# Kernel tuning notes

Hardware: AMD Instinct MI355X
Metric: run time of the kernel (lower is better)

Reference implementation:

```python
import jax, jax.numpy as jnp
import numpy as np

N_NODES = 100000
N_EDGES = 1600000
IN_DIM = 128
HID = 128
OUT_DIM = 64
N_LAYERS = 2
MAXK = 16


def setup_inputs() -> dict:
    key = jax.random.key(0)
    ks = jax.random.split(key, 8)
    x = jax.random.normal(ks[0], (N_NODES, IN_DIM), dtype=jnp.float32)
    src = jax.random.randint(ks[1], (N_EDGES,), 0, N_NODES, dtype=jnp.int32)
    dst = jax.random.randint(ks[2], (N_EDGES,), 0, N_NODES, dtype=jnp.int32)
    # Linear weights stored as [in, out] (y = x @ W + b), xavier-like scale
    s_in = float(np.sqrt(2.0 / (IN_DIM + HID)))
    s_h = float(np.sqrt(2.0 / (HID + HID)))
    s_out = float(np.sqrt(2.0 / (HID + OUT_DIM)))
    W_in = jax.random.normal(ks[3], (IN_DIM, HID), dtype=jnp.float32) * s_in
    b_in = jnp.zeros((HID,), dtype=jnp.float32)
    W_lin = jax.random.normal(ks[4], (N_LAYERS, HID, HID), dtype=jnp.float32) * s_h
    b_lin = jnp.zeros((N_LAYERS, HID), dtype=jnp.float32)
    eps = jnp.zeros((N_LAYERS,), dtype=jnp.float32)  # learn_eps=True, init_eps=0
    W_out = jax.random.normal(ks[5], (HID, OUT_DIM), dtype=jnp.float32) * s_out
    b_out = jnp.zeros((OUT_DIM,), dtype=jnp.float32)
    return {"x": x, "src": src, "dst": dst, "W_in": W_in, "b_in": b_in,
            "W_lin": W_lin, "b_lin": b_lin, "eps": eps,
            "W_out": W_out, "b_out": b_out}


def _maxk(x, k):
    # OPTMaxK: keep top-k entries per row (dim=1), zero the rest.
    _, idx = jax.lax.top_k(x, k)                      # [N, k]
    rows = jnp.arange(x.shape[0])[:, None]            # [N, 1]
    mask = jnp.zeros_like(x).at[rows, idx].set(1.0)
    return x * mask


def reference(x, src, dst, W_in, b_in, W_lin, b_lin, eps, W_out, b_out):
    n = x.shape[0]
    h = jax.nn.relu(x @ W_in + b_in)                  # lin_in + relu
    for i in range(N_LAYERS):
        h = h @ W_lin[i] + b_lin[i]                   # per-layer Linear
        h_sparse = _maxk(h, MAXK)                     # MaxK nonlinearity (dropout p=0 -> identity)
        # GIN sum aggregation over edges: neigh[v] = sum_{(u->v)} h_sparse[u]
        msg = jnp.take(h_sparse, src, axis=0)         # [E, HID] irregular gather
        neigh = jax.ops.segment_sum(msg, dst, num_segments=n)
        h = (1.0 + eps[i]) * h_sparse + neigh         # eps residual (apply_func=None, no norm)
    return h @ W_out + b_out
```

## Files before the change

kernel.cpp:

```cpp
#include <hip/hip_runtime.h>
#include <cstdint>
#include <cstddef>


typedef __attribute__((ext_vector_type(8))) short bf16x8;
typedef __attribute__((ext_vector_type(4))) float f32x4;

#define BSHIFT 8
#define NBUK 512

__device__ __forceinline__ unsigned rne_bf16(float v) {
  unsigned u = __float_as_uint(v);
  return (u + 0x7fffu + ((u >> 16) & 1u)) >> 16;
}

__device__ __forceinline__ void row_select16(
    const float v[8], int row, int nrows, int shift, int s, unsigned below,
    unsigned char* __restrict__ Cs, float* __restrict__ Vs) {
  unsigned k[8];
#pragma unroll
  for (int j = 0; j < 8; ++j) {
    const unsigned u = __float_as_uint(v[j]);
    k[j] = u ^ (((unsigned)((int)u >> 31)) | 0x80000000u);
  }

  unsigned P = 0;
  int kth = 16;
  int sz = 128;
  bool done = false;
  for (int b = 31; b >= 0; --b) {
    const unsigned tgt = (P >> b) | 1u;
    int c = 0;
#pragma unroll
    for (int j = 0; j < 8; ++j) {
      const unsigned long long bal = __ballot((k[j] >> b) == tgt);
      c += __popc((unsigned)((bal >> shift) & 0xFFFFull));
    }
    if (!done) {
      if (c >= kth) {
        P |= (1u << b);
        sz = c;
      } else {
        sz -= c;
        kth -= c;
      }
      done = (sz == kth);
    }
    if (__all(done)) break;
  }
  if (done) P -= 1u;

  unsigned gtm[8], eqm[8];
  int gt_total = 0;
#pragma unroll
  for (int j = 0; j < 8; ++j) {
    const unsigned long long gb = __ballot(k[j] > P);
    const unsigned long long eb = __ballot(k[j] == P);
    gtm[j] = (unsigned)((gb >> shift) & 0xFFFFull);
    eqm[j] = (unsigned)((eb >> shift) & 0xFFFFull);
    gt_total += __popc(gtm[j]);
  }
  const int need = 16 - gt_total;
  int gt_pre = 0, eq_pre = 0;
#pragma unroll
  for (int j = 0; j < 8; ++j) {
    const bool isgt = k[j] > P;
    const bool iseq = k[j] == P;
    const int gtb = gt_pre + __popc(gtm[j] & below);
    const int eqb = eq_pre + __popc(eqm[j] & below);
    if (row < nrows && (isgt || (iseq && eqb < need))) {
      const int rank = gtb + (isgt ? min(eqb, need) : eqb);
      Vs[(size_t)row * 16 + rank] = v[j];
      Cs[(size_t)row * 16 + rank] = (unsigned char)(j * 16 + s);
    }
    gt_pre += __popc(gtm[j]);
    eq_pre += __popc(eqm[j]);
  }
}

__global__ __launch_bounds__(256) void wt_build_all_kernel(
    const float* __restrict__ W_in, const float* __restrict__ W_lin,
    const float* __restrict__ W_out, short* __restrict__ out) {
  const int i = blockIdx.x * 256 + threadIdx.x;
  if (i >= 57344) return;
  const float* W;
  int nout, local;
  short* H;
  if (i < 16384) {
    W = W_in; nout = 128; local = i; H = out;
  } else if (i < 32768) {
    W = W_lin; nout = 128; local = i - 16384; H = out + 32768;
  } else if (i < 49152) {
    W = W_lin + 16384; nout = 128; local = i - 32768; H = out + 65536;
  } else {
    W = W_out; nout = 64; local = i - 49152; H = out + 98304;
  }
  const int nn = local >> 7, k = local & 127;
  const float v = W[k * nout + nn];
  const unsigned hb = rne_bf16(v);
  const float hf = __uint_as_float(hb << 16);
  const unsigned lb = rne_bf16(v - hf);
  H[local] = (short)hb;
  H[local + nout * 128] = (short)lb;
}

__global__ __launch_bounds__(256, 2) void gemm_in_kernel(
    const float* __restrict__ X, const short* __restrict__ WtH,
    const short* __restrict__ WtL, const float* __restrict__ bias,
    short* __restrict__ Yh, short* __restrict__ Yl, int nrows, int ntiles) {
  constexpr int NOUT = 128;
  constexpr int NT = NOUT / 16;
  constexpr int LDB = 128 * 2 + 16;
  constexpr int PLANE = NOUT * LDB;
  __shared__ char lds[2 * PLANE];

  const int tid = threadIdx.x;
  for (int u = tid; u < 2 * NOUT * 16; u += 256) {
    const int plane = u / (NOUT * 16);
    const int v = u % (NOUT * 16);
    const int nrow = v >> 4, seg = v & 15;
    const short* src = plane ? WtL : WtH;
    const float4 d = *(const float4*)&src[nrow * 128 + seg * 8];
    *(float4*)&lds[plane * PLANE + nrow * LDB + seg * 16] = d;
  }
  __syncthreads();

  const int lane = tid & 63;
  const int wv = tid >> 6;
  const int li = lane & 15;
  const int kg = lane >> 4;

  float bv[NT];
#pragma unroll
  for (int t = 0; t < NT; ++t) bv[t] = bias[t * 16 + li];

  for (int tile = blockIdx.x; tile < ntiles; tile += gridDim.x) {
    const int rowbase = tile * 256 + wv * 64;

    f32x4 acc[4][NT];
#pragma unroll
    for (int rg = 0; rg < 4; ++rg)
#pragma unroll
      for (int t = 0; t < NT; ++t) acc[rg][t] = (f32x4){0.f, 0.f, 0.f, 0.f};

#pragma unroll
    for (int c = 0; c < 4; ++c) {
      bf16x8 ah[4], al[4];
#pragma unroll
      for (int rg = 0; rg < 4; ++rg) {
        const int row = rowbase + rg * 16 + li;
        const int rowc = (row < nrows) ? row : (nrows - 1);
        const float* xrow = X + (size_t)rowc * 128 + c * 32 + kg * 8;
        const float4 p0 = *(const float4*)&xrow[0];
        const float4 p1 = *(const float4*)&xrow[4];
        const float f[8] = {p0.x, p0.y, p0.z, p0.w, p1.x, p1.y, p1.z, p1.w};
#pragma unroll
        for (int e = 0; e < 8; ++e) {
          const unsigned hb = rne_bf16(f[e]);
          const float hf = __uint_as_float(hb << 16);
          ah[rg][e] = (short)hb;
          al[rg][e] = (short)rne_bf16(f[e] - hf);
        }
      }
      const int kb = c * 64 + kg * 16;
#pragma unroll
      for (int t = 0; t < NT; ++t) {
        const int boff = (t * 16 + li) * LDB + kb;
        const bf16x8 bh = *(const bf16x8*)&lds[boff];
        const bf16x8 bl = *(const bf16x8*)&lds[PLANE + boff];
#pragma unroll
        for (int rg = 0; rg < 4; ++rg) {
          acc[rg][t] =
              __builtin_amdgcn_mfma_f32_16x16x32_bf16(al[rg], bh, acc[rg][t], 0, 0, 0);
          acc[rg][t] =
              __builtin_amdgcn_mfma_f32_16x16x32_bf16(ah[rg], bl, acc[rg][t], 0, 0, 0);
          acc[rg][t] =
              __builtin_amdgcn_mfma_f32_16x16x32_bf16(ah[rg], bh, acc[rg][t], 0, 0, 0);
        }
      }
    }

#pragma unroll
    for (int rg = 0; rg < 4; ++rg) {
      const int orow = rowbase + rg * 16 + kg * 4;
#pragma unroll
      for (int t = 0; t < NT; ++t) {
        const int col = t * 16 + li;
#pragma unroll
        for (int r = 0; r < 4; ++r) {
          const int rr = orow + r;
          if (rr < nrows) {
            const float o = fmaxf(acc[rg][t][r] + bv[t], 0.f);
            const unsigned hb = rne_bf16(o);
            const float hf = __uint_as_float(hb << 16);
            Yh[(size_t)rr * 128 + col] = (short)hb;
            Yl[(size_t)rr * 128 + col] = (short)rne_bf16(o - hf);
          }
        }
      }
    }
  }
}

__global__ __launch_bounds__(256, 2) void gemm_maxk_kernel(
    const short* __restrict__ Xh, const short* __restrict__ Xl,
    const short* __restrict__ WtH, const short* __restrict__ WtL,
    const float* __restrict__ bias, unsigned char* __restrict__ Cs,
    float* __restrict__ Vs, int nrows, int ntiles) {
  constexpr int NOUT = 128;
  constexpr int NT = NOUT / 16;
  constexpr int LDB = 128 * 2 + 16;
  constexpr int PLANE = NOUT * LDB;
  __shared__ char lds[2 * PLANE];

  const int tid = threadIdx.x;
  for (int u = tid; u < 2 * NOUT * 16; u += 256) {
    const int plane = u / (NOUT * 16);
    const int v = u % (NOUT * 16);
    const int nrow = v >> 4, seg = v & 15;
    const short* src = plane ? WtL : WtH;
    const float4 d = *(const float4*)&src[nrow * 128 + seg * 8];
    *(float4*)&lds[plane * PLANE + nrow * LDB + seg * 16] = d;
  }
  __syncthreads();

  const int lane = tid & 63;
  const int wv = tid >> 6;
  const int li = lane & 15;
  const int kg = lane >> 4;
  const int shift = kg * 16;
  const unsigned below = (1u << li) - 1u;

  float bv[NT];
#pragma unroll
  for (int t = 0; t < NT; ++t) bv[t] = bias[t * 16 + li];

  for (int tile = blockIdx.x; tile < ntiles; tile += gridDim.x) {
    const int rowbase = tile * 256 + wv * 64;

    f32x4 acc[4][NT];
#pragma unroll
    for (int rg = 0; rg < 4; ++rg)
#pragma unroll
      for (int t = 0; t < NT; ++t) acc[rg][t] = (f32x4){0.f, 0.f, 0.f, 0.f};

#pragma unroll
    for (int c = 0; c < 4; ++c) {
      bf16x8 ah[4], al[4];
#pragma unroll
      for (int rg = 0; rg < 4; ++rg) {
        const int row = rowbase + rg * 16 + li;
        const int rowc = (row < nrows) ? row : (nrows - 1);
        ah[rg] = *(const bf16x8*)&Xh[(size_t)rowc * 128 + c * 32 + kg * 8];
        al[rg] = *(const bf16x8*)&Xl[(size_t)rowc * 128 + c * 32 + kg * 8];
      }
      const int kb = c * 64 + kg * 16;
#pragma unroll
      for (int t = 0; t < NT; ++t) {
        const int boff = (t * 16 + li) * LDB + kb;
        const bf16x8 bh = *(const bf16x8*)&lds[boff];
        const bf16x8 bl = *(const bf16x8*)&lds[PLANE + boff];
#pragma unroll
        for (int rg = 0; rg < 4; ++rg) {
          acc[rg][t] =
              __builtin_amdgcn_mfma_f32_16x16x32_bf16(al[rg], bh, acc[rg][t], 0, 0, 0);
          acc[rg][t] =
              __builtin_amdgcn_mfma_f32_16x16x32_bf16(ah[rg], bl, acc[rg][t], 0, 0, 0);
          acc[rg][t] =
              __builtin_amdgcn_mfma_f32_16x16x32_bf16(ah[rg], bh, acc[rg][t], 0, 0, 0);
        }
      }
    }

#pragma unroll
    for (int rg = 0; rg < 4; ++rg) {
#pragma unroll
      for (int r = 0; r < 4; ++r) {
        const int row = rowbase + rg * 16 + kg * 4 + r;
        float v[8];
#pragma unroll
        for (int t = 0; t < NT; ++t) v[t] = acc[rg][t][r] + bv[t];
        row_select16(v, row, nrows, shift, li, below, Cs, Vs);
      }
    }
  }
}

template <int NOUT>
__global__ __launch_bounds__(256, 2) void gemm_pl_kernel(
    const short* __restrict__ Xh, const short* __restrict__ Xl,
    const short* __restrict__ WtH, const short* __restrict__ WtL,
    const float* __restrict__ bias, float* __restrict__ Y, int nrows,
    int ntiles) {
  constexpr int NT = NOUT / 16;
  constexpr int LDB = 128 * 2 + 16;
  constexpr int PLANE = NOUT * LDB;
  __shared__ char lds[2 * PLANE];

  const int tid = threadIdx.x;
  for (int u = tid; u < 2 * NOUT * 16; u += 256) {
    const int plane = u / (NOUT * 16);
    const int v = u % (NOUT * 16);
    const int nrow = v >> 4, seg = v & 15;
    const short* src = plane ? WtL : WtH;
    const float4 d = *(const float4*)&src[nrow * 128 + seg * 8];
    *(float4*)&lds[plane * PLANE + nrow * LDB + seg * 16] = d;
  }
  __syncthreads();

  const int lane = tid & 63;
  const int wv = tid >> 6;
  const int li = lane & 15;
  const int kg = lane >> 4;

  float bv[NT];
#pragma unroll
  for (int t = 0; t < NT; ++t) bv[t] = bias[t * 16 + li];

  for (int tile = blockIdx.x; tile < ntiles; tile += gridDim.x) {
    const int rowbase = tile * 256 + wv * 64;

    f32x4 acc[4][NT];
#pragma unroll
    for (int rg = 0; rg < 4; ++rg)
#pragma unroll
      for (int t = 0; t < NT; ++t) acc[rg][t] = (f32x4){0.f, 0.f, 0.f, 0.f};

#pragma unroll
    for (int c = 0; c < 4; ++c) {
      bf16x8 ah[4], al[4];
#pragma unroll
      for (int rg = 0; rg < 4; ++rg) {
        const int row = rowbase + rg * 16 + li;
        const int rowc = (row < nrows) ? row : (nrows - 1);
        ah[rg] = *(const bf16x8*)&Xh[(size_t)rowc * 128 + c * 32 + kg * 8];
        al[rg] = *(const bf16x8*)&Xl[(size_t)rowc * 128 + c * 32 + kg * 8];
      }
      const int kb = c * 64 + kg * 16;
#pragma unroll
      for (int t = 0; t < NT; ++t) {
        const int boff = (t * 16 + li) * LDB + kb;
        const bf16x8 bh = *(const bf16x8*)&lds[boff];
        const bf16x8 bl = *(const bf16x8*)&lds[PLANE + boff];
#pragma unroll
        for (int rg = 0; rg < 4; ++rg) {
          acc[rg][t] =
              __builtin_amdgcn_mfma_f32_16x16x32_bf16(al[rg], bh, acc[rg][t], 0, 0, 0);
          acc[rg][t] =
              __builtin_amdgcn_mfma_f32_16x16x32_bf16(ah[rg], bl, acc[rg][t], 0, 0, 0);
          acc[rg][t] =
              __builtin_amdgcn_mfma_f32_16x16x32_bf16(ah[rg], bh, acc[rg][t], 0, 0, 0);
        }
      }
    }

#pragma unroll
    for (int rg = 0; rg < 4; ++rg) {
      const int orow = rowbase + rg * 16 + kg * 4;
#pragma unroll
      for (int t = 0; t < NT; ++t) {
        const int col = t * 16 + li;
#pragma unroll
        for (int r = 0; r < 4; ++r) {
          const int rr = orow + r;
          if (rr < nrows) Y[(size_t)rr * NOUT + col] = acc[rg][t][r] + bv[t];
        }
      }
    }
  }
}

__global__ __launch_bounds__(256) void bhist_kernel(const int* __restrict__ dst,
                                                    int* __restrict__ BC,
                                                    int E) {
  __shared__ int bh[NBUK];
  for (int i = threadIdx.x; i < NBUK; i += 256) bh[i] = 0;
  __syncthreads();
  const int stride = gridDim.x * 256;
  for (int e = blockIdx.x * 256 + threadIdx.x; e < E; e += stride)
    atomicAdd(&bh[dst[e] >> BSHIFT], 1);
  __syncthreads();
  for (int i = threadIdx.x; i < NBUK; i += 256)
    if (bh[i]) atomicAdd(&BC[i], bh[i]);
}

__global__ __launch_bounds__(NBUK) void bscan_kernel(
    const int* __restrict__ BC, int* __restrict__ bases,
    int* __restrict__ bcur, int* __restrict__ rs, int n, int E) {
  __shared__ int sc[NBUK];
  const int t = threadIdx.x;
  const int c = BC[t];
  sc[t] = c;
  __syncthreads();
  for (int st = 1; st < NBUK; st <<= 1) {
    const int v = sc[t];
    const int u = (t >= st) ? sc[t - st] : 0;
    __syncthreads();
    sc[t] = v + u;
    __syncthreads();
  }
  const int excl = sc[t] - c;
  bases[t] = excl;
  bcur[t] = excl;
  if (t == 0) rs[n] = E;
}

__global__ __launch_bounds__(256) void bin_kernel(
    const int* __restrict__ src, const int* __restrict__ dst,
    int* __restrict__ bcur, uint2* __restrict__ binned, int E, int chunk) {
  __shared__ int cnt[NBUK], off[NBUK], gbase[NBUK];
  __shared__ unsigned short bktof[4096];
  __shared__ uint2 buf[4096];
  const int t = threadIdx.x;
  const int beg = blockIdx.x * chunk;
  const int m = min(chunk, E - beg);
  if (m <= 0) return;

  for (int i = t; i < NBUK; i += 256) cnt[i] = 0;
  __syncthreads();

  int d[16], s[16], lp[16], bk[16];
#pragma unroll
  for (int i = 0; i < 16; ++i) {
    const int j = i * 256 + t;
    if (j < m) {
      d[i] = dst[beg + j];
      s[i] = src[beg + j];
      bk[i] = d[i] >> BSHIFT;
      lp[i] = atomicAdd(&cnt[bk[i]], 1);
    } else {
      bk[i] = -1;
    }
  }
  __syncthreads();

  for (int i = t; i < NBUK; i += 256) off[i] = cnt[i];
  __syncthreads();
  for (int st = 1; st < NBUK; st <<= 1) {
    int v0, v1, u0, u1;
    {
      const int i0 = t, i1 = t + 256;
      v0 = off[i0]; u0 = (i0 >= st) ? off[i0 - st] : 0;
      v1 = off[i1]; u1 = (i1 >= st) ? off[i1 - st] : 0;
    }
    __syncthreads();
    off[t] = v0 + u0;
    off[t + 256] = v1 + u1;
    __syncthreads();
  }

  for (int i = t; i < NBUK; i += 256) {
    const int c = cnt[i];
    if (c > 0) {
      gbase[i] = atomicAdd(&bcur[i], c);
      const int e0 = off[i] - c;
      for (int k = 0; k < c; ++k) bktof[e0 + k] = (unsigned short)i;
    }
  }
  __syncthreads();

#pragma unroll
  for (int i = 0; i < 16; ++i) {
    if (bk[i] >= 0) {
      buf[(off[bk[i]] - cnt[bk[i]]) + lp[i]] =
          make_uint2((unsigned)d[i], (unsigned)s[i]);
    }
  }
  __syncthreads();

  for (int j = t; j < m; j += 256) {
    const int b = bktof[j];
    const int e0 = off[b] - cnt[b];
    binned[gbase[b] + (j - e0)] = buf[j];
  }
}

__global__ __launch_bounds__(256) void bbuild_kernel(
    const int* __restrict__ bases, const int* __restrict__ BC,
    const uint2* __restrict__ binned, int* __restrict__ rs,
    int* __restrict__ csr_src, int n) {
  __shared__ int nd[256], sc[256], cur[256];
  const int b = blockIdx.x;
  const int t = threadIdx.x;
  const int base = bases[b];
  const int count = BC[b];
  const int node0 = b << BSHIFT;

  nd[t] = 0;
  __syncthreads();
  for (int i = t; i < count; i += 256)
    atomicAdd(&nd[binned[base + i].x & 255], 1);
  __syncthreads();

  sc[t] = nd[t];
  __syncthreads();
  for (int st = 1; st < 256; st <<= 1) {
    const int v = sc[t];
    const int u = (t >= st) ? sc[t - st] : 0;
    __syncthreads();
    sc[t] = v + u;
    __syncthreads();
  }
  const int excl = sc[t] - nd[t];
  cur[t] = excl;
  if (node0 + t < n) rs[node0 + t] = base + excl;
  __syncthreads();

  for (int i = t; i < count; i += 256) {
    const uint2 p = binned[base + i];
    const int pos = atomicAdd(&cur[p.x & 255], 1);
    csr_src[base + pos] = (int)p.y;
  }
}

__global__ __launch_bounds__(256) void gather6_kernel(
    const int* __restrict__ rs, const int* __restrict__ csr_src,
    const unsigned char* __restrict__ Cs, const float* __restrict__ Vs,
    const float* __restrict__ eps_p, short* __restrict__ Ah,
    short* __restrict__ Al, int nrows) {
  __shared__ __align__(16) float sv[4][16][16];
  __shared__ __align__(16) unsigned char scb[4][16][16];
  __shared__ float accb[4][4 * 132];
  const int lane = threadIdx.x & 63;
  const int wid = threadIdx.x >> 6;
  const float e1 = 1.0f + *eps_p;
  const int ee = lane >> 2;
  const int q = lane & 3;
  const int g = lane >> 4;
  const int p = lane & 15;
  float* acc = accb[wid];
  float4* acc4 = (float4*)acc;

  for (int r = blockIdx.x * 4 + wid; r < nrows; r += gridDim.x * 4) {
    for (int i = lane; i < 132; i += 64)
      acc4[i] = make_float4(0.f, 0.f, 0.f, 0.f);

    const int beg = rs[r], end = rs[r + 1];
    for (int base = beg; base < end; base += 16) {
      const int cnt = min(16, end - base);
      if (ee < cnt) {
        const int s = csr_src[base + ee];
        if (q == 0) {
          const int4 c4 = *(const int4*)&Cs[(size_t)s * 16];
          *(int4*)&scb[wid][ee][0] = c4;
        }
        const float4 v = *(const float4*)&Vs[(size_t)s * 16 + q * 4];
        *(float4*)&sv[wid][ee][q * 4] = v;
      }
      for (int e = 0; e < cnt; e += 4) {
        const int eg = e + g;
        if (eg < cnt) {
          const int col = scb[wid][eg][p];
          const float val = sv[wid][eg][p];
          acc[g * 132 + col] += val;
        }
      }
    }
    if (lane < 16) {
      const int c = Cs[(size_t)r * 16 + lane];
      const float v = Vs[(size_t)r * 16 + lane];
      acc[c] += e1 * v;
    }
    const float a0 = acc[lane] + acc[132 + lane] + acc[264 + lane] +
                     acc[396 + lane];
    const float a1 = acc[64 + lane] + acc[132 + 64 + lane] +
                     acc[264 + 64 + lane] + acc[396 + 64 + lane];
    const unsigned h0 = rne_bf16(a0);
    const unsigned h1 = rne_bf16(a1);
    Ah[(size_t)r * 128 + lane] = (short)h0;
    Ah[(size_t)r * 128 + 64 + lane] = (short)h1;
    Al[(size_t)r * 128 + lane] =
        (short)rne_bf16(a0 - __uint_as_float(h0 << 16));
    Al[(size_t)r * 128 + 64 + lane] =
        (short)rne_bf16(a1 - __uint_as_float(h1 << 16));
  }
}

extern "C" void kernel_launch(void* const* d_in, const int* in_sizes, int n_in,
                              void* d_out, int out_size, void* d_ws,
                              size_t ws_size, hipStream_t stream) {
  const float* x = (const float*)d_in[0];
  const int* src = (const int*)d_in[1];
  const int* dst = (const int*)d_in[2];
  const float* W_in = (const float*)d_in[3];
  const float* b_in = (const float*)d_in[4];
  const float* W_lin = (const float*)d_in[5];
  const float* b_lin = (const float*)d_in[6];
  const float* eps = (const float*)d_in[7];
  const float* W_out = (const float*)d_in[8];
  const float* b_out = (const float*)d_in[9];
  float* out = (float*)d_out;

  const int n = in_sizes[0] / 128;
  const int E = in_sizes[1];

  char* w = (char*)d_ws;
  unsigned char* Cs = (unsigned char*)w; w += (size_t)n * 16;
  float* Vs = (float*)w;              w += (size_t)n * 16 * 4;
  int* rs = (int*)w;                  w += (size_t)(n + 1) * 4;
  int* csr_src = (int*)w;             w += (size_t)E * 4;
  uint2* binned = (uint2*)w;          w += (size_t)E * 8;
  int* BC = (int*)w;                  w += NBUK * 4;
  int* bases = (int*)w;               w += NBUK * 4;
  int* bcur = (int*)w;                w += NBUK * 4;
  short* wtAll = (short*)w;           w += (size_t)114688 * 2;
  short* Ah = (short*)w;              w += (size_t)n * 128 * 2;
  short* Al = (short*)w;              w += (size_t)n * 128 * 2;

  short* wtIn = wtAll;
  short* wtL0 = wtAll + 32768;
  short* wtL1 = wtAll + 65536;
  short* wtOut = wtAll + 98304;

  const int ptiles = (n + 255) / 256;
  const int nbuk_eff = (n + 255) >> BSHIFT;
  const int chunk = 4000;
  const int cblocks = (E + chunk - 1) / chunk;
  const dim3 blk(256);

  hipMemsetAsync(BC, 0, NBUK * 4, stream);
  bhist_kernel<<<256, blk, 0, stream>>>(dst, BC, E);
  bscan_kernel<<<1, NBUK, 0, stream>>>(BC, bases, bcur, rs, n, E);
  bin_kernel<<<cblocks, blk, 0, stream>>>(src, dst, bcur, binned, E, chunk);
  bbuild_kernel<<<nbuk_eff, blk, 0, stream>>>(bases, BC, binned, rs, csr_src,
                                              n);

  wt_build_all_kernel<<<(57344 + 255) / 256, blk, 0, stream>>>(W_in, W_lin,
                                                               W_out, wtAll);

  gemm_in_kernel<<<ptiles, blk, 0, stream>>>(x, wtIn, wtIn + 16384, b_in, Ah,
                                             Al, n, ptiles);

  for (int l = 0; l < 2; ++l) {
    short* wt = l ? wtL1 : wtL0;
    gemm_maxk_kernel<<<ptiles, blk, 0, stream>>>(
        Ah, Al, wt, wt + 16384, b_lin + (size_t)l * 128, Cs, Vs, n, ptiles);
    gather6_kernel<<<2048, blk, 0, stream>>>(rs, csr_src, Cs, Vs, eps + l, Ah,
                                             Al, n);
  }

  gemm_pl_kernel<64><<<ptiles, blk, 0, stream>>>(Ah, Al, wtOut, wtOut + 8192,
                                                 b_out, out, n, ptiles);
}
```

Measured before the change: 441.9 us.

## Split fused GEMM+MaxK into separate GEMM and standalone top-k select kernels

Replaces the fused per-layer GEMM with in-register top-16 selection by a plain GEMM that writes a full fp32 activation buffer, followed by a dedicated maxk_kernel that reads it back and performs the ballot-based radix select. Layer 1 uses a new 512-thread GEMM variant with 32 rows per wave. The aim is to free the GEMM from the register pressure and divergence of the select loop and run selection at its own occupancy. In exchange it adds an extra kernel launch and an n×128 fp32 round trip through global memory per layer.

```diff
diff --git a/kernel.cpp b/kernel.cpp
--- a/kernel.cpp
+++ b/kernel.cpp
@@ -12,70 +12,6 @@
 __device__ __forceinline__ unsigned rne_bf16(float v) {
   unsigned u = __float_as_uint(v);
   return (u + 0x7fffu + ((u >> 16) & 1u)) >> 16;
-}
-
-__device__ __forceinline__ void row_select16(
-    const float v[8], int row, int nrows, int shift, int s, unsigned below,
-    unsigned char* __restrict__ Cs, float* __restrict__ Vs) {
-  unsigned k[8];
-#pragma unroll
-  for (int j = 0; j < 8; ++j) {
-    const unsigned u = __float_as_uint(v[j]);
-    k[j] = u ^ (((unsigned)((int)u >> 31)) | 0x80000000u);
-  }
-
-  unsigned P = 0;
-  int kth = 16;
-  int sz = 128;
-  bool done = false;
-  for (int b = 31; b >= 0; --b) {
-    const unsigned tgt = (P >> b) | 1u;
-    int c = 0;
-#pragma unroll
-    for (int j = 0; j < 8; ++j) {
-      const unsigned long long bal = __ballot((k[j] >> b) == tgt);
-      c += __popc((unsigned)((bal >> shift) & 0xFFFFull));
-    }
-    if (!done) {
-      if (c >= kth) {
-        P |= (1u << b);
-        sz = c;
-      } else {
-        sz -= c;
-        kth -= c;
-      }
-      done = (sz == kth);
-    }
-    if (__all(done)) break;
-  }
-  if (done) P -= 1u;
-
-  unsigned gtm[8], eqm[8];
-  int gt_total = 0;
-#pragma unroll
-  for (int j = 0; j < 8; ++j) {
-    const unsigned long long gb = __ballot(k[j] > P);
-    const unsigned long long eb = __ballot(k[j] == P);
-    gtm[j] = (unsigned)((gb >> shift) & 0xFFFFull);
-    eqm[j] = (unsigned)((eb >> shift) & 0xFFFFull);
-    gt_total += __popc(gtm[j]);
-  }
-  const int need = 16 - gt_total;
-  int gt_pre = 0, eq_pre = 0;
-#pragma unroll
-  for (int j = 0; j < 8; ++j) {
-    const bool isgt = k[j] > P;
-    const bool iseq = k[j] == P;
-    const int gtb = gt_pre + __popc(gtm[j] & below);
-    const int eqb = eq_pre + __popc(eqm[j] & below);
-    if (row < nrows && (isgt || (iseq && eqb < need))) {
-      const int rank = gtb + (isgt ? min(eqb, need) : eqb);
-      Vs[(size_t)row * 16 + rank] = v[j];
-      Cs[(size_t)row * 16 + rank] = (unsigned char)(j * 16 + s);
-    }
-    gt_pre += __popc(gtm[j]);
-    eq_pre += __popc(eqm[j]);
-  }
 }
 
 __global__ __launch_bounds__(256) void wt_build_all_kernel(
@@ -165,9 +101,8 @@
       const int kb = c * 64 + kg * 16;
 #pragma unroll
       for (int t = 0; t < NT; ++t) {
-        const int boff = (t * 16 + li) * LDB + kb;
-        const bf16x8 bh = *(const bf16x8*)&lds[boff];
-        const bf16x8 bl = *(const bf16x8*)&lds[PLANE + boff];
+        const bf16x8 bh = *(const bf16x8*)&lds[(t * 16 + li) * LDB + kb];
+        const bf16x8 bl = *(const bf16x8*)&lds[PLANE + (t * 16 + li) * LDB + kb];
 #pragma unroll
         for (int rg = 0; rg < 4; ++rg) {
           acc[rg][t] =
@@ -197,90 +132,6 @@
             Yl[(size_t)rr * 128 + col] = (short)rne_bf16(o - hf);
           }
         }
-      }
-    }
-  }
-}
-
-__global__ __launch_bounds__(256, 2) void gemm_maxk_kernel(
-    const short* __restrict__ Xh, const short* __restrict__ Xl,
-    const short* __restrict__ WtH, const short* __restrict__ WtL,
-    const float* __restrict__ bias, unsigned char* __restrict__ Cs,
-    float* __restrict__ Vs, int nrows, int ntiles) {
-  constexpr int NOUT = 128;
-  constexpr int NT = NOUT / 16;
-  constexpr int LDB = 128 * 2 + 16;
-  constexpr int PLANE = NOUT * LDB;
-  __shared__ char lds[2 * PLANE];
-
-  const int tid = threadIdx.x;
-  for (int u = tid; u < 2 * NOUT * 16; u += 256) {
-    const int plane = u / (NOUT * 16);
-    const int v = u % (NOUT * 16);
-    const int nrow = v >> 4, seg = v & 15;
-    const short* src = plane ? WtL : WtH;
-    const float4 d = *(const float4*)&src[nrow * 128 + seg * 8];
-    *(float4*)&lds[plane * PLANE + nrow * LDB + seg * 16] = d;
-  }
-  __syncthreads();
-
-  const int lane = tid & 63;
-  const int wv = tid >> 6;
-  const int li = lane & 15;
-  const int kg = lane >> 4;
-  const int shift = kg * 16;
-  const unsigned below = (1u << li) - 1u;
-
-  float bv[NT];
-#pragma unroll
-  for (int t = 0; t < NT; ++t) bv[t] = bias[t * 16 + li];
-
-  for (int tile = blockIdx.x; tile < ntiles; tile += gridDim.x) {
-    const int rowbase = tile * 256 + wv * 64;
-
-    f32x4 acc[4][NT];
-#pragma unroll
-    for (int rg = 0; rg < 4; ++rg)
-#pragma unroll
-      for (int t = 0; t < NT; ++t) acc[rg][t] = (f32x4){0.f, 0.f, 0.f, 0.f};
-
-#pragma unroll
-    for (int c = 0; c < 4; ++c) {
-      bf16x8 ah[4], al[4];
-#pragma unroll
-      for (int rg = 0; rg < 4; ++rg) {
-        const int row = rowbase + rg * 16 + li;
-        const int rowc = (row < nrows) ? row : (nrows - 1);
-        ah[rg] = *(const bf16x8*)&Xh[(size_t)rowc * 128 + c * 32 + kg * 8];
-        al[rg] = *(const bf16x8*)&Xl[(size_t)rowc * 128 + c * 32 + kg * 8];
-      }
-      const int kb = c * 64 + kg * 16;
-#pragma unroll
-      for (int t = 0; t < NT; ++t) {
-        const int boff = (t * 16 + li) * LDB + kb;
-        const bf16x8 bh = *(const bf16x8*)&lds[boff];
-        const bf16x8 bl = *(const bf16x8*)&lds[PLANE + boff];
-#pragma unroll
-        for (int rg = 0; rg < 4; ++rg) {
-          acc[rg][t] =
-              __builtin_amdgcn_mfma_f32_16x16x32_bf16(al[rg], bh, acc[rg][t], 0, 0, 0);
-          acc[rg][t] =
-              __builtin_amdgcn_mfma_f32_16x16x32_bf16(ah[rg], bl, acc[rg][t], 0, 0, 0);
-          acc[rg][t] =
-              __builtin_amdgcn_mfma_f32_16x16x32_bf16(ah[rg], bh, acc[rg][t], 0, 0, 0);
-        }
-      }
-    }
-
-#pragma unroll
-    for (int rg = 0; rg < 4; ++rg) {
-#pragma unroll
-      for (int r = 0; r < 4; ++r) {
-        const int row = rowbase + rg * 16 + kg * 4 + r;
-        float v[8];
-#pragma unroll
-        for (int t = 0; t < NT; ++t) v[t] = acc[rg][t][r] + bv[t];
-        row_select16(v, row, nrows, shift, li, below, Cs, Vs);
       }
     }
   }
@@ -339,9 +190,8 @@
       const int kb = c * 64 + kg * 16;
 #pragma unroll
       for (int t = 0; t < NT; ++t) {
-        const int boff = (t * 16 + li) * LDB + kb;
-        const bf16x8 bh = *(const bf16x8*)&lds[boff];
-        const bf16x8 bl = *(const bf16x8*)&lds[PLANE + boff];
+        const bf16x8 bh = *(const bf16x8*)&lds[(t * 16 + li) * LDB + kb];
+        const bf16x8 bl = *(const bf16x8*)&lds[PLANE + (t * 16 + li) * LDB + kb];
 #pragma unroll
         for (int rg = 0; rg < 4; ++rg) {
           acc[rg][t] =
@@ -366,6 +216,169 @@
           if (rr < nrows) Y[(size_t)rr * NOUT + col] = acc[rg][t][r] + bv[t];
         }
       }
+    }
+  }
+}
+
+__global__ __launch_bounds__(512, 2) void gemm_pl8_kernel(
+    const short* __restrict__ Xh, const short* __restrict__ Xl,
+    const short* __restrict__ WtH, const short* __restrict__ WtL,
+    const float* __restrict__ bias, float* __restrict__ Y, int nrows,
+    int ntiles) {
+  constexpr int NOUT = 128;
+  constexpr int NT = NOUT / 16;
+  constexpr int LDB = 128 * 2 + 16;
+  constexpr int PLANE = NOUT * LDB;
+  __shared__ char lds[2 * PLANE];
+
+  const int tid = threadIdx.x;
+  for (int u = tid; u < 2 * NOUT * 16; u += 512) {
+    const int plane = u / (NOUT * 16);
+    const int v = u % (NOUT * 16);
+    const int nrow = v >> 4, seg = v & 15;
+    const short* src = plane ? WtL : WtH;
+    const float4 d = *(const float4*)&src[nrow * 128 + seg * 8];
+    *(float4*)&lds[plane * PLANE + nrow * LDB + seg * 16] = d;
+  }
+  __syncthreads();
+
+  const int lane = tid & 63;
+  const int wv = tid >> 6;
+  const int li = lane & 15;
+  const int kg = lane >> 4;
+
+  float bv[NT];
+#pragma unroll
+  for (int t = 0; t < NT; ++t) bv[t] = bias[t * 16 + li];
+
+  for (int tile = blockIdx.x; tile < ntiles; tile += gridDim.x) {
+    const int rowbase = tile * 256 + wv * 32;
+
+    f32x4 acc[2][NT];
+#pragma unroll
+    for (int rg = 0; rg < 2; ++rg)
+#pragma unroll
+      for (int t = 0; t < NT; ++t) acc[rg][t] = (f32x4){0.f, 0.f, 0.f, 0.f};
+
+#pragma unroll
+    for (int c = 0; c < 4; ++c) {
+      bf16x8 ah[2], al[2];
+#pragma unroll
+      for (int rg = 0; rg < 2; ++rg) {
+        const int row = rowbase + rg * 16 + li;
+        const int rowc = (row < nrows) ? row : (nrows - 1);
+        ah[rg] = *(const bf16x8*)&Xh[(size_t)rowc * 128 + c * 32 + kg * 8];
+        al[rg] = *(const bf16x8*)&Xl[(size_t)rowc * 128 + c * 32 + kg * 8];
+      }
+      const int kb = c * 64 + kg * 16;
+#pragma unroll
+      for (int t = 0; t < NT; ++t) {
+        const bf16x8 bh = *(const bf16x8*)&lds[(t * 16 + li) * LDB + kb];
+        const bf16x8 bl = *(const bf16x8*)&lds[PLANE + (t * 16 + li) * LDB + kb];
+#pragma unroll
+        for (int rg = 0; rg < 2; ++rg) {
+          acc[rg][t] =
+              __builtin_amdgcn_mfma_f32_16x16x32_bf16(al[rg], bh, acc[rg][t], 0, 0, 0);
+          acc[rg][t] =
+              __builtin_amdgcn_mfma_f32_16x16x32_bf16(ah[rg], bl, acc[rg][t], 0, 0, 0);
+          acc[rg][t] =
+              __builtin_amdgcn_mfma_f32_16x16x32_bf16(ah[rg], bh, acc[rg][t], 0, 0, 0);
+        }
+      }
+    }
+
+#pragma unroll
+    for (int rg = 0; rg < 2; ++rg) {
+      const int orow = rowbase + rg * 16 + kg * 4;
+#pragma unroll
+      for (int t = 0; t < NT; ++t) {
+        const int col = t * 16 + li;
+#pragma unroll
+        for (int r = 0; r < 4; ++r) {
+          const int rr = orow + r;
+          if (rr < nrows) Y[(size_t)rr * NOUT + col] = acc[rg][t][r] + bv[t];
+        }
+      }
+    }
+  }
+}
+
+__global__ __launch_bounds__(256) void maxk_kernel(
+    const float* __restrict__ T, unsigned char* __restrict__ Cs,
+    float* __restrict__ Vs, int nrows) {
+  const int lane = threadIdx.x & 63;
+  const int wid = threadIdx.x >> 6;
+  const int sub = lane >> 4;
+  const int s = lane & 15;
+  const int shift = sub * 16;
+  const unsigned below = (1u << s) - 1u;
+  const int nquads = (nrows + 3) / 4;
+
+  for (int quad = blockIdx.x * 4 + wid; quad < nquads; quad += gridDim.x * 4) {
+    const int row = quad * 4 + sub;
+    const int rowc = (row < nrows) ? row : (nrows - 1);
+    const float* Trow = T + (size_t)rowc * 128;
+
+    float v[8];
+    unsigned k[8];
+#pragma unroll
+    for (int j = 0; j < 8; ++j) {
+      v[j] = Trow[j * 16 + s];
+      const unsigned u = __float_as_uint(v[j]);
+      k[j] = u ^ (((unsigned)((int)u >> 31)) | 0x80000000u);
+    }
+
+    unsigned P = 0;
+    int kth = 16;
+    int sz = 128;
+    bool done = false;
+    for (int b = 31; b >= 0; --b) {
+      const unsigned tgt = (P >> b) | 1u;
+      int c = 0;
+#pragma unroll
+      for (int j = 0; j < 8; ++j) {
+        const unsigned long long bal = __ballot((k[j] >> b) == tgt);
+        c += __popc((unsigned)((bal >> shift) & 0xFFFFull));
+      }
+      if (!done) {
+        if (c >= kth) {
+          P |= (1u << b);
+          sz = c;
+        } else {
+          sz -= c;
+          kth -= c;
+        }
+        done = (sz == kth);
+      }
+      if (__all(done)) break;
+    }
+    if (done) P -= 1u;
+
+    unsigned gtm[8], eqm[8];
+    int gt_total = 0;
+#pragma unroll
+    for (int j = 0; j < 8; ++j) {
+      const unsigned long long gb = __ballot(k[j] > P);
+      const unsigned long long eb = __ballot(k[j] == P);
+      gtm[j] = (unsigned)((gb >> shift) & 0xFFFFull);
+      eqm[j] = (unsigned)((eb >> shift) & 0xFFFFull);
+      gt_total += __popc(gtm[j]);
+    }
+    const int need = 16 - gt_total;
+    int gt_pre = 0, eq_pre = 0;
+#pragma unroll
+    for (int j = 0; j < 8; ++j) {
+      const bool isgt = k[j] > P;
+      const bool iseq = k[j] == P;
+      const int gtb = gt_pre + __popc(gtm[j] & below);
+      const int eqb = eq_pre + __popc(eqm[j] & below);
+      if (row < nrows && (isgt || (iseq && eqb < need))) {
+        const int rank = gtb + (isgt ? min(eqb, need) : eqb);
+        Vs[(size_t)row * 16 + rank] = v[j];
+        Cs[(size_t)row * 16 + rank] = (unsigned char)(j * 16 + s);
+      }
+      gt_pre += __popc(gtm[j]);
+      eq_pre += __popc(eqm[j]);
     }
   }
 }
@@ -595,6 +608,7 @@
   const int E = in_sizes[1];
 
   char* w = (char*)d_ws;
+  float* B = (float*)w;               w += (size_t)n * 128 * 4;
   unsigned char* Cs = (unsigned char*)w; w += (size_t)n * 16;
   float* Vs = (float*)w;              w += (size_t)n * 16 * 4;
   int* rs = (int*)w;                  w += (size_t)(n + 1) * 4;
@@ -633,8 +647,14 @@
 
   for (int l = 0; l < 2; ++l) {
     short* wt = l ? wtL1 : wtL0;
-    gemm_maxk_kernel<<<ptiles, blk, 0, stream>>>(
-        Ah, Al, wt, wt + 16384, b_lin + (size_t)l * 128, Cs, Vs, n, ptiles);
+    if (l == 0) {
+      gemm_pl_kernel<128><<<ptiles, blk, 0, stream>>>(
+          Ah, Al, wt, wt + 16384, b_lin, B, n, ptiles);
+    } else {
+      gemm_pl8_kernel<<<ptiles, dim3(512), 0, stream>>>(
+          Ah, Al, wt, wt + 16384, b_lin + 128, B, n, ptiles);
+    }
+    maxk_kernel<<<2048, blk, 0, stream>>>(B, Cs, Vs, n);
     gather6_kernel<<<2048, blk, 0, stream>>>(rs, csr_src, Cs, Vs, eps + l, Ah,
                                              Al, n);
   }
```

Result: faster. 425.4 us (-3.7%).
